# Optimization experiments

Measured on AMD Instinct MI355X. Metric: run time of the kernel, lower is better.

## Reference

```python
import jax, jax.numpy as jnp
import numpy as np

K = 4          # neighbors
R = 2          # step_ratio
OUT = 64       # output_size

def knn_idx(x, k):
    # x: (B, C, N) -> indices of k nearest neighbors (incl. self): (B, N, k)
    xx = jnp.sum(x * x, axis=1)                       # (B, N)
    inner = jnp.einsum('bcn,bcm->bnm', x, x)          # (B, N, N)
    neg_dist = 2.0 * inner - xx[:, :, None] - xx[:, None, :]
    _, idx = jax.lax.top_k(neg_dist, k)               # largest neg_dist = nearest
    return idx

def setup_inputs() -> dict:
    key = jax.random.key(0)
    ks = jax.random.split(key, 7)
    B, C, N = 16, 64, 2048
    s = 0.05
    return {
        'x':  jax.random.normal(ks[0], (B, C, N), jnp.float32),
        'w1': jax.random.normal(ks[1], (OUT, 2 * C), jnp.float32) * s,
        'b1': jax.random.normal(ks[2], (OUT,), jnp.float32) * s,
        'w2': jax.random.normal(ks[3], (OUT * R, 2 * C + OUT), jnp.float32) * s,
        'b2': jax.random.normal(ks[4], (OUT * R,), jnp.float32) * s,
        'w3': jax.random.normal(ks[5], (OUT, OUT), jnp.float32) * s,
        'b3': jax.random.normal(ks[6], (OUT,), jnp.float32) * s,
    }

def reference(x, w1, b1, w2, b2, w3, b3):
    B, C, N = x.shape
    idx = knn_idx(x, K)                                # (B, N, K)
    xt = jnp.transpose(x, (0, 2, 1))                   # (B, N, C)
    neighbors = xt[jnp.arange(B)[:, None, None], idx]  # (B, N, K, C)
    center = jnp.broadcast_to(xt[:, :, None, :], neighbors.shape)
    feat = jnp.concatenate([center, neighbors], axis=-1)   # (B, N, K, 2C), minus_center=False
    # get_graph_feature returns (B, 2C, N, K); module permutes to (B, 2C, K, N)
    f = jnp.transpose(feat, (0, 3, 2, 1))              # (B, 2C, K, N)
    e1 = jnp.einsum('oc,bckn->bokn', w1, f) + b1[None, :, None, None]
    e = jax.nn.relu(jnp.concatenate([e1, f], axis=1))  # (B, 2C+OUT, K, N)
    e2 = jax.nn.relu(jnp.einsum('oc,bckn->bokn', w2, e) + b2[None, :, None, None])  # (B, OUT*R, K, N)
    # permute(0,2,3,1) -> (B,K,N,OUT*R), view -> (B,K,N*R,OUT), permute -> (B,OUT,K,N*R)
    e2 = jnp.transpose(e2, (0, 2, 3, 1)).reshape(B, K, N * R, OUT)
    e2 = jnp.transpose(e2, (0, 3, 1, 2))               # (B, OUT, K, N*R)
    e3 = jnp.einsum('oc,bckn->bokn', w3, e2) + b3[None, :, None, None]
    return jnp.max(e3, axis=2)                          # (B, OUT, N*R)
```

## Files before the change

kernel.cpp:

```cpp
#include <hip/hip_runtime.h>
#include <hip/hip_bf16.h>

#define BB 16
#define CC 64
#define NN 2048
#define KK 4
#define NPART 4
#define JPER (NN / NPART)
#define NCAND 32
#define RSTRIDE 80

typedef unsigned short u16;
typedef unsigned int u32;
typedef __attribute__((ext_vector_type(4))) float f32x4;
typedef __attribute__((ext_vector_type(16))) float f32x16;
typedef __attribute__((ext_vector_type(8))) short short8;

__device__ __forceinline__ float bf2f(u16 u) {
    unsigned int x = ((unsigned int)u) << 16;
    float f;
    __builtin_memcpy(&f, &x, 4);
    return f;
}
__device__ __forceinline__ u16 f2bf(float f) {
    __hip_bfloat16 h = __float2bfloat16(f);
    u16 u;
    __builtin_memcpy(&u, &h, 2);
    return u;
}
__device__ __forceinline__ unsigned int pk2(float a, float b) {
    return (unsigned int)f2bf(a) | ((unsigned int)f2bf(b) << 16);
}
__device__ __forceinline__ u32 umx(u32 a, u32 b) { return a > b ? a : b; }
__device__ __forceinline__ u32 umn(u32 a, u32 b) { return a < b ? a : b; }

__global__ __launch_bounds__(256) void k_prep(const float* __restrict__ x,
                                              float* __restrict__ xt,
                                              double* __restrict__ xx64,
                                              u16* __restrict__ xpk) {
    int b = blockIdx.y;
    int n = blockIdx.x * 256 + threadIdx.x;
    const float* xb = x + (size_t)b * CC * NN;
    float v[CC];
    float s = 0.f;
    double s64 = 0.0;
#pragma unroll
    for (int c = 0; c < CC; c++) {
        v[c] = xb[(size_t)c * NN + n];
        s = fmaf(v[c], v[c], s);
        s64 += (double)v[c] * (double)v[c];
    }
    float4* dst = (float4*)(xt + ((size_t)b * NN + n) * CC);
#pragma unroll
    for (int q = 0; q < 16; q++) {
        dst[q] = make_float4(v[4 * q], v[4 * q + 1], v[4 * q + 2], v[4 * q + 3]);
    }
    xx64[b * NN + n] = s64;
    u16* dp = xpk + ((size_t)b * NN + n) * RSTRIDE;
#pragma unroll
    for (int q = 0; q < 8; q++) {
        uint4 u;
        u.x = pk2(v[8 * q], v[8 * q + 1]);
        u.y = pk2(v[8 * q + 2], v[8 * q + 3]);
        u.z = pk2(v[8 * q + 4], v[8 * q + 5]);
        u.w = pk2(v[8 * q + 6], v[8 * q + 7]);
        *(uint4*)(dp + q * 8) = u;
    }
    u16 hi = f2bf(s);
    u16 lo = f2bf(s - bf2f(hi));
    uint4 u8;
    u8.x = (unsigned int)hi | ((unsigned int)lo << 16);
    u8.y = 0x00003F80u;
    u8.z = 0; u8.w = 0;
    *(uint4*)(dp + 64) = u8;
    uint4 z = {0, 0, 0, 0};
    *(uint4*)(dp + 72) = z;
}

__global__ __launch_bounds__(256) void k_wprep(const float* __restrict__ w1,
                                               const float* __restrict__ w2,
                                               const float* __restrict__ w3,
                                               u16* __restrict__ wb1,
                                               u16* __restrict__ wb2,
                                               u16* __restrict__ wb3) {
    int t = blockIdx.x * 256 + threadIdx.x;
    int stride = gridDim.x * 256;
    for (int idx = t; idx < 64 * 128; idx += stride) {
        int o = idx >> 7, k = idx & 127;
        int cb = o >> 4, lr = o & 15, ks = k >> 5, g = (k >> 3) & 3, e = k & 7;
        wb1[((cb * 4 + ks) * 64 + g * 16 + lr) * 8 + e] = f2bf(w1[idx]);
    }
    for (int idx = t; idx < 128 * 192; idx += stride) {
        int o = idx / 192, k = idx - o * 192;
        int cb = o >> 4, lr = o & 15, ks = k >> 5, g = (k >> 3) & 3, e = k & 7;
        wb2[((cb * 6 + ks) * 64 + g * 16 + lr) * 8 + e] = f2bf(w2[idx]);
    }
    for (int idx = t; idx < 64 * 64; idx += stride) {
        int o = idx >> 6, k = idx & 63;
        int cb = o >> 4, lr = o & 15, ks = k >> 5, g = (k >> 3) & 3, e = k & 7;
        wb3[((cb * 2 + ks) * 64 + g * 16 + lr) * 8 + e] = f2bf(w3[idx]);
    }
}

__global__ __launch_bounds__(256) void k_knn3(const u16* __restrict__ xpk,
                                              u16* __restrict__ cand) {
    int ib = blockIdx.x;
    int part = blockIdx.y;
    int b = blockIdx.z;
    int tid = threadIdx.x;
    int i0 = ib * 128;
    int j00 = part * JPER;

    __shared__ u16 Bb[2 * 2 * 10 * 32 * 8];

    int w = tid >> 6, l = tid & 63;
    int lc = l & 31, lh = l >> 5;
    int hb4 = lh * 4;

    short8 ifrag[5];
    {
        const u16* ip = xpk + ((size_t)b * NN + i0 + w * 32 + lc) * RSTRIDE + lh * 8;
#pragma unroll
        for (int ks = 0; ks < 4; ks++) ifrag[ks] = *(const short8*)(ip + ks * 16);
        short8 f4 = {0, 0, 0, 0, 0, 0, 0, 0};
        if (lh == 0) {
            f4[0] = (short)0xBF00;
            f4[1] = (short)0xBF00;
            f4[2] = (short)0x4300;
        }
        ifrag[4] = f4;
    }

    u32 v0 = 0, v1 = 0, v2 = 0, v3 = 0;

#define CE(a, b) { u32 mx_ = umx(a, b); b = umn(a, b); a = mx_; }

#define STAGE(rr, bf)                                                              \
    {                                                                              \
        int jb = j00 + (rr) * 64;                                                  \
        for (int g = tid; g < 640; g += 256) {                                     \
            int rw = g / 10, c = g - rw * 10;                                      \
            uint4 u = *(const uint4*)(xpk + ((size_t)b * NN + jb + rw) * RSTRIDE + \
                                      c * 8);                                      \
            int sub = rw >> 5, r32 = rw & 31;                                      \
            *(uint4*)((char*)Bb + (bf) * 10240 + sub * 5120 + c * 512 +            \
                      ((r32 ^ (c & 7)) * 16)) = u;                                 \
        }                                                                          \
    }

    STAGE(0, 0);

    for (int r = 0; r < JPER / 64; r++) {
        __syncthreads();
        if (r + 1 < JPER / 64) STAGE(r + 1, (r + 1) & 1);

        const char* bufp = (const char*)Bb + (r & 1) * 10240;
        f32x16 acc0, acc1;
#pragma unroll
        for (int e = 0; e < 16; e++) {
            acc0[e] = 0.f;
            acc1[e] = 0.f;
        }
#pragma unroll
        for (int ks = 0; ks < 5; ks++) {
            int c = ks * 2 + lh;
            int boff = c * 512 + ((lc ^ (c & 7)) * 16);
            short8 a0 = *(const short8*)(bufp + boff);
            short8 a1 = *(const short8*)(bufp + 5120 + boff);
            acc0 = __builtin_amdgcn_mfma_f32_32x32x16_bf16(a0, ifrag[ks], acc0, 0, 0, 0);
            acc1 = __builtin_amdgcn_mfma_f32_32x32x16_bf16(a1, ifrag[ks], acc1, 0, 0, 0);
        }
#pragma unroll
        for (int sub = 0; sub < 2; sub++) {
            const f32x16& acc = sub ? acc1 : acc0;
            int jlb = r * 64 + sub * 32 + hb4;
            u32 kk[16];
#pragma unroll
            for (int rg = 0; rg < 16; rg++) {
                u32 u;
                float f = acc[rg];
                __builtin_memcpy(&u, &f, 4);
                int coff = (rg & 3) + 8 * (rg >> 2);
                kk[rg] = (u & ~0x1FFu) | (u32)(jlb + coff);
            }
#pragma unroll
            for (int q = 0; q < 4; q++) {
                int p = q * 4;
                CE(kk[p + 0], kk[p + 2]); CE(kk[p + 1], kk[p + 3]);
                CE(kk[p + 0], kk[p + 1]); CE(kk[p + 2], kk[p + 3]);
                CE(kk[p + 1], kk[p + 2]);
            }
            kk[0] = umx(kk[0], kk[7]); kk[1] = umx(kk[1], kk[6]);
            kk[2] = umx(kk[2], kk[5]); kk[3] = umx(kk[3], kk[4]);
            CE(kk[0], kk[2]); CE(kk[1], kk[3]); CE(kk[0], kk[1]); CE(kk[2], kk[3]);
            kk[8] = umx(kk[8], kk[15]); kk[9] = umx(kk[9], kk[14]);
            kk[10] = umx(kk[10], kk[13]); kk[11] = umx(kk[11], kk[12]);
            CE(kk[8], kk[10]); CE(kk[9], kk[11]); CE(kk[8], kk[9]); CE(kk[10], kk[11]);
            kk[0] = umx(kk[0], kk[11]); kk[1] = umx(kk[1], kk[10]);
            kk[2] = umx(kk[2], kk[9]); kk[3] = umx(kk[3], kk[8]);
            CE(kk[0], kk[2]); CE(kk[1], kk[3]); CE(kk[0], kk[1]); CE(kk[2], kk[3]);
            v0 = umx(v0, kk[3]); v1 = umx(v1, kk[2]);
            v2 = umx(v2, kk[1]); v3 = umx(v3, kk[0]);
            CE(v0, v2); CE(v1, v3); CE(v0, v1); CE(v2, v3);
        }
    }
#undef STAGE
#undef CE

    size_t cb = ((size_t)b * NN + i0 + w * 32 + lc) * NCAND + part * 8 + lh * 4;
    cand[cb + 0] = (u16)(j00 + (v0 & 0x1FF));
    cand[cb + 1] = (u16)(j00 + (v1 & 0x1FF));
    cand[cb + 2] = (u16)(j00 + (v2 & 0x1FF));
    cand[cb + 3] = (u16)(j00 + (v3 & 0x1FF));
}

__global__ __launch_bounds__(256) void k_knn_merge(const float* __restrict__ xt,
                                                   const double* __restrict__ xx64,
                                                   const u16* __restrict__ cand,
                                                   int* __restrict__ nidx) {
    __shared__ double sv[16 * 33];
    __shared__ u16 ji[16 * 33];

    int tid = threadIdx.x;
    int g = tid >> 4;
    int q = tid & 15;
    size_t gp0 = (size_t)blockIdx.x * 16;
    size_t bbase = (gp0 >> 11) << 11;

    for (int idx = tid; idx < 16 * 32; idx += 256) {
        int p = idx >> 5, c = idx & 31;
        ji[p * 33 + c] = cand[(gp0 + p) * NCAND + c];
    }
    __syncthreads();

    float4 a = ((const float4*)(xt + (gp0 + g) * CC))[q];

    for (int c0 = 0; c0 < NCAND; c0 += 4) {
        int j0 = ji[g * 33 + c0 + 0];
        int j1 = ji[g * 33 + c0 + 1];
        int j2 = ji[g * 33 + c0 + 2];
        int j3 = ji[g * 33 + c0 + 3];
        float4 b0 = ((const float4*)(xt + (bbase + j0) * CC))[q];
        float4 b1 = ((const float4*)(xt + (bbase + j1) * CC))[q];
        float4 b2 = ((const float4*)(xt + (bbase + j2) * CC))[q];
        float4 b3 = ((const float4*)(xt + (bbase + j3) * CC))[q];
        double d0 = (double)a.x * b0.x + (double)a.y * b0.y +
                    (double)a.z * b0.z + (double)a.w * b0.w;
        double d1 = (double)a.x * b1.x + (double)a.y * b1.y +
                    (double)a.z * b1.z + (double)a.w * b1.w;
        double d2 = (double)a.x * b2.x + (double)a.y * b2.y +
                    (double)a.z * b2.z + (double)a.w * b2.w;
        double d3 = (double)a.x * b3.x + (double)a.y * b3.y +
                    (double)a.z * b3.z + (double)a.w * b3.w;
        d0 += __shfl_xor(d0, 8); d1 += __shfl_xor(d1, 8);
        d2 += __shfl_xor(d2, 8); d3 += __shfl_xor(d3, 8);
        d0 += __shfl_xor(d0, 4); d1 += __shfl_xor(d1, 4);
        d2 += __shfl_xor(d2, 4); d3 += __shfl_xor(d3, 4);
        d0 += __shfl_xor(d0, 2); d1 += __shfl_xor(d1, 2);
        d2 += __shfl_xor(d2, 2); d3 += __shfl_xor(d3, 2);
        d0 += __shfl_xor(d0, 1); d1 += __shfl_xor(d1, 1);
        d2 += __shfl_xor(d2, 1); d3 += __shfl_xor(d3, 1);
        if (q == 0) {
            sv[g * 33 + c0 + 0] = 2.0 * d0 - xx64[bbase + j0];
            sv[g * 33 + c0 + 1] = 2.0 * d1 - xx64[bbase + j1];
            sv[g * 33 + c0 + 2] = 2.0 * d2 - xx64[bbase + j2];
            sv[g * 33 + c0 + 3] = 2.0 * d3 - xx64[bbase + j3];
        }
    }
    __syncthreads();

    if (tid < 16) {
        int p = tid;
        double v4[4];
        int id4[4];
#pragma unroll
        for (int s = 0; s < 4; s++) {
            v4[s] = -1e300;
            id4[s] = 0x7fffffff;
        }
        for (int cc = 0; cc < NCAND; cc++) {
            double cv = sv[p * 33 + cc];
            int ci = ji[p * 33 + cc];
#pragma unroll
            for (int s = 0; s < 4; s++) {
                bool take = (cv > v4[s]) || (cv == v4[s] && ci < id4[s]);
                double nv = take ? cv : v4[s];
                int ni = take ? ci : id4[s];
                double ov = take ? v4[s] : cv;
                int oi = take ? id4[s] : ci;
                v4[s] = nv;
                id4[s] = ni;
                cv = ov;
                ci = oi;
            }
        }
        size_t gp2 = gp0 + p;
#pragma unroll
        for (int s = 0; s < 4; s++) nidx[gp2 * 4 + s] = id4[s];
    }
}

__global__ __launch_bounds__(256) void k_mlp(const u16* __restrict__ xpk,
                                             const int* __restrict__ nidx,
                                             const u16* __restrict__ wb1,
                                             const u16* __restrict__ wb2,
                                             const u16* __restrict__ wb3,
                                             const float* __restrict__ b1,
                                             const float* __restrict__ b2,
                                             const float* __restrict__ b3,
                                             float* __restrict__ out) {
    int nch = blockIdx.x;
    int b = blockIdx.y;
    int n0 = nch * 16;
    int tid = threadIdx.x;

    __shared__ u16 Fb[64 * 128];
    __shared__ u16 E1b[64 * 64];
    __shared__ u16 E2b[64 * 128];
    __shared__ float Ob[64 * 36];
    __shared__ int ji[64];

    if (tid < 64) ji[tid] = nidx[((size_t)b * NN + n0) * KK + tid];
    __syncthreads();

    for (int g = tid; g < 64 * 16; g += 256) {
        int it = g >> 4, q = g & 15;
        int half = q >> 3, cq = q & 7;
        int srcn = half ? ji[it] : (n0 + (it >> 2));
        uint4 u = *(const uint4*)(xpk + ((size_t)b * NN + srcn) * RSTRIDE + cq * 8);
        int byte = (it * 256 + half * 128 + cq * 16) ^ ((it & 7) << 4);
        *(uint4*)((char*)Fb + byte) = u;
    }
    __syncthreads();

    int w = tid >> 6, l = tid & 63;
    int lr = l & 15, lg = l >> 4;

    {
        f32x4 acc[4];
#pragma unroll
        for (int g = 0; g < 4; g++) acc[g] = (f32x4){0.f, 0.f, 0.f, 0.f};
#pragma unroll
        for (int ks = 0; ks < 4; ks++) {
            short8 bw = *(const short8*)(wb1 + ((size_t)(w * 4 + ks) * 64 + l) * 8);
#pragma unroll
            for (int g = 0; g < 4; g++) {
                int arow = g * 16 + lr;
                int off = (arow * 256 + ks * 64 + lg * 16) ^ ((arow & 7) << 4);
                short8 a = *(const short8*)((const char*)Fb + off);
                acc[g] = __builtin_amdgcn_mfma_f32_16x16x32_bf16(a, bw, acc[g], 0, 0, 0);
            }
        }
        float bias = b1[w * 16 + lr];
#pragma unroll
        for (int g = 0; g < 4; g++) {
#pragma unroll
            for (int q = 0; q < 4; q++) {
                int item = g * 16 + lg * 4 + q;
                float vv = fmaxf(acc[g][q] + bias, 0.f);
                int byte = (item * 128 + (w * 16 + lr) * 2) ^ ((item & 7) << 4);
                *(u16*)((char*)E1b + byte) = f2bf(vv);
            }
        }
    }
    __syncthreads();

    {
        f32x4 acc[4][2];
#pragma unroll
        for (int g = 0; g < 4; g++)
#pragma unroll
            for (int c2 = 0; c2 < 2; c2++) acc[g][c2] = (f32x4){0.f, 0.f, 0.f, 0.f};
#pragma unroll
        for (int ks = 0; ks < 6; ks++) {
            short8 bw0 = *(const short8*)(wb2 + ((size_t)((w * 2) * 6 + ks) * 64 + l) * 8);
            short8 bw1 = *(const short8*)(wb2 + ((size_t)((w * 2 + 1) * 6 + ks) * 64 + l) * 8);
#pragma unroll
            for (int g = 0; g < 4; g++) {
                int arow = g * 16 + lr;
                int aswz = (arow & 7) << 4;
                short8 a;
                if (ks < 2) {
                    int off = (arow * 128 + ks * 64 + lg * 16) ^ aswz;
                    a = *(const short8*)((const char*)E1b + off);
                } else {
                    int off = (arow * 256 + (ks - 2) * 64 + lg * 16) ^ aswz;
                    uint4 u = *(const uint4*)((const char*)Fb + off);
                    unsigned int m;
                    m = ((u.x >> 15) & 0x10001u) * 0xFFFFu; u.x &= ~m;
                    m = ((u.y >> 15) & 0x10001u) * 0xFFFFu; u.y &= ~m;
                    m = ((u.z >> 15) & 0x10001u) * 0xFFFFu; u.z &= ~m;
                    m = ((u.w >> 15) & 0x10001u) * 0xFFFFu; u.w &= ~m;
                    __builtin_memcpy(&a, &u, 16);
                }
                acc[g][0] = __builtin_amdgcn_mfma_f32_16x16x32_bf16(a, bw0, acc[g][0], 0, 0, 0);
                acc[g][1] = __builtin_amdgcn_mfma_f32_16x16x32_bf16(a, bw1, acc[g][1], 0, 0, 0);
            }
        }
#pragma unroll
        for (int c2 = 0; c2 < 2; c2++) {
            float bias = b2[(w * 2 + c2) * 16 + lr];
#pragma unroll
            for (int g = 0; g < 4; g++) {
#pragma unroll
                for (int q = 0; q < 4; q++) {
                    int item = g * 16 + lg * 4 + q;
                    float vv = fmaxf(acc[g][c2][q] + bias, 0.f);
                    int byte = (item * 256 + ((w * 2 + c2) * 16 + lr) * 2) ^ ((item & 7) << 4);
                    *(u16*)((char*)E2b + byte) = f2bf(vv);
                }
            }
        }
    }
    __syncthreads();

    {
        f32x4 acc[4][2];
#pragma unroll
        for (int g = 0; g < 4; g++)
#pragma unroll
            for (int r = 0; r < 2; r++) acc[g][r] = (f32x4){0.f, 0.f, 0.f, 0.f};
#pragma unroll
        for (int ks = 0; ks < 2; ks++) {
            short8 bw = *(const short8*)(wb3 + ((size_t)(w * 2 + ks) * 64 + l) * 8);
#pragma unroll
            for (int g = 0; g < 4; g++) {
                int arow = g * 16 + lr;
                int aswz = (arow & 7) << 4;
#pragma unroll
                for (int r = 0; r < 2; r++) {
                    int off = (arow * 256 + r * 128 + ks * 64 + lg * 16) ^ aswz;
                    short8 a = *(const short8*)((const char*)E2b + off);
                    acc[g][r] = __builtin_amdgcn_mfma_f32_16x16x32_bf16(a, bw, acc[g][r], 0, 0, 0);
                }
            }
        }
        float bias = b3[w * 16 + lr];
        int o = w * 16 + lr;
#pragma unroll
        for (int g = 0; g < 4; g++) {
            int nl = g * 4 + lg;
#pragma unroll
            for (int r = 0; r < 2; r++) {
                float m = fmaxf(fmaxf(acc[g][r][0], acc[g][r][1]),
                                fmaxf(acc[g][r][2], acc[g][r][3])) + bias;
                Ob[o * 36 + nl * 2 + r] = m;
            }
        }
    }
    __syncthreads();

    {
        int o = tid >> 2, q = tid & 3;
        float4 v0 = *(const float4*)&Ob[o * 36 + q * 8];
        float4 v1 = *(const float4*)&Ob[o * 36 + q * 8 + 4];
        float* dst = out + ((size_t)(b * 64 + o)) * 4096 + n0 * 2 + q * 8;
        ((float4*)dst)[0] = v0;
        ((float4*)dst)[1] = v1;
    }
}

extern "C" void kernel_launch(void* const* d_in, const int* in_sizes, int n_in,
                              void* d_out, int out_size, void* d_ws, size_t ws_size,
                              hipStream_t stream) {
    const float* x = (const float*)d_in[0];
    const float* w1 = (const float*)d_in[1];
    const float* b1 = (const float*)d_in[2];
    const float* w2 = (const float*)d_in[3];
    const float* b2 = (const float*)d_in[4];
    const float* w3 = (const float*)d_in[5];
    const float* b3 = (const float*)d_in[6];
    float* out = (float*)d_out;

    float* xt = (float*)d_ws;
    u16* xpk = (u16*)(xt + (size_t)BB * NN * CC);
    double* xx64 = (double*)(xpk + (size_t)BB * NN * RSTRIDE);
    int* nidx = (int*)(xx64 + (size_t)BB * NN);
    u16* cand = (u16*)(nidx + (size_t)BB * NN * KK);
    u16* wb1 = cand + (size_t)BB * NN * NCAND;
    u16* wb2 = wb1 + 64 * 128;
    u16* wb3 = wb2 + 128 * 192;

    k_prep<<<dim3(NN / 256, BB), 256, 0, stream>>>(x, xt, xx64, xpk);
    k_wprep<<<dim3(32), 256, 0, stream>>>(w1, w2, w3, wb1, wb2, wb3);
    k_knn3<<<dim3(NN / 128, NPART, BB), 256, 0, stream>>>(xpk, cand);
    k_knn_merge<<<dim3(BB * NN / 16), 256, 0, stream>>>(xt, xx64, cand, nidx);
    k_mlp<<<dim3(NN / 16, BB), 256, 0, stream>>>(xpk, nidx, wb1, wb2, wb3, b1, b2, b3, out);
}
```

Baseline: 114.9 us.

## Fuse kNN candidate merge into MLP kernel and swizzle block order

The separate kNN merge kernel is folded into the start of the MLP kernel. Each block refines its own 16 points' candidates in double precision, reusing the Fb shared buffer for the scratch values, and keeps the final 4 neighbor indices in shared memory. This removes one kernel launch and the global round trip through the nidx buffer. The block index is also remapped so that consecutive blocks spread across batches, which may change cache locality. In exchange, the MLP blocks now carry the merge's latency-bound gather and the single-threaded top-4 selection serially before their MLP work.

```diff
diff --git a/kernel.cpp b/kernel.cpp
--- a/kernel.cpp
+++ b/kernel.cpp
@@ -214,119 +214,116 @@
     cand[cb + 3] = (u16)(j00 + (v3 & 0x1FF));
 }
 
-__global__ __launch_bounds__(256) void k_knn_merge(const float* __restrict__ xt,
-                                                   const double* __restrict__ xx64,
-                                                   const u16* __restrict__ cand,
-                                                   int* __restrict__ nidx) {
-    __shared__ double sv[16 * 33];
-    __shared__ u16 ji[16 * 33];
-
+__global__ __launch_bounds__(256) void k_mmlp(const float* __restrict__ xt,
+                                              const double* __restrict__ xx64,
+                                              const u16* __restrict__ cand,
+                                              const u16* __restrict__ xpk,
+                                              const u16* __restrict__ wb1,
+                                              const u16* __restrict__ wb2,
+                                              const u16* __restrict__ wb3,
+                                              const float* __restrict__ b1,
+                                              const float* __restrict__ b2,
+                                              const float* __restrict__ b3,
+                                              float* __restrict__ out) {
     int tid = threadIdx.x;
-    int g = tid >> 4;
-    int q = tid & 15;
-    size_t gp0 = (size_t)blockIdx.x * 16;
-    size_t bbase = (gp0 >> 11) << 11;
-
-    for (int idx = tid; idx < 16 * 32; idx += 256) {
-        int p = idx >> 5, c = idx & 31;
-        ji[p * 33 + c] = cand[(gp0 + p) * NCAND + c];
-    }
-    __syncthreads();
-
-    float4 a = ((const float4*)(xt + (gp0 + g) * CC))[q];
-
-    for (int c0 = 0; c0 < NCAND; c0 += 4) {
-        int j0 = ji[g * 33 + c0 + 0];
-        int j1 = ji[g * 33 + c0 + 1];
-        int j2 = ji[g * 33 + c0 + 2];
-        int j3 = ji[g * 33 + c0 + 3];
-        float4 b0 = ((const float4*)(xt + (bbase + j0) * CC))[q];
-        float4 b1 = ((const float4*)(xt + (bbase + j1) * CC))[q];
-        float4 b2 = ((const float4*)(xt + (bbase + j2) * CC))[q];
-        float4 b3 = ((const float4*)(xt + (bbase + j3) * CC))[q];
-        double d0 = (double)a.x * b0.x + (double)a.y * b0.y +
-                    (double)a.z * b0.z + (double)a.w * b0.w;
-        double d1 = (double)a.x * b1.x + (double)a.y * b1.y +
-                    (double)a.z * b1.z + (double)a.w * b1.w;
-        double d2 = (double)a.x * b2.x + (double)a.y * b2.y +
-                    (double)a.z * b2.z + (double)a.w * b2.w;
-        double d3 = (double)a.x * b3.x + (double)a.y * b3.y +
-                    (double)a.z * b3.z + (double)a.w * b3.w;
-        d0 += __shfl_xor(d0, 8); d1 += __shfl_xor(d1, 8);
-        d2 += __shfl_xor(d2, 8); d3 += __shfl_xor(d3, 8);
-        d0 += __shfl_xor(d0, 4); d1 += __shfl_xor(d1, 4);
-        d2 += __shfl_xor(d2, 4); d3 += __shfl_xor(d3, 4);
-        d0 += __shfl_xor(d0, 2); d1 += __shfl_xor(d1, 2);
-        d2 += __shfl_xor(d2, 2); d3 += __shfl_xor(d3, 2);
-        d0 += __shfl_xor(d0, 1); d1 += __shfl_xor(d1, 1);
-        d2 += __shfl_xor(d2, 1); d3 += __shfl_xor(d3, 1);
-        if (q == 0) {
-            sv[g * 33 + c0 + 0] = 2.0 * d0 - xx64[bbase + j0];
-            sv[g * 33 + c0 + 1] = 2.0 * d1 - xx64[bbase + j1];
-            sv[g * 33 + c0 + 2] = 2.0 * d2 - xx64[bbase + j2];
-            sv[g * 33 + c0 + 3] = 2.0 * d3 - xx64[bbase + j3];
-        }
-    }
-    __syncthreads();
-
-    if (tid < 16) {
-        int p = tid;
-        double v4[4];
-        int id4[4];
-#pragma unroll
-        for (int s = 0; s < 4; s++) {
-            v4[s] = -1e300;
-            id4[s] = 0x7fffffff;
-        }
-        for (int cc = 0; cc < NCAND; cc++) {
-            double cv = sv[p * 33 + cc];
-            int ci = ji[p * 33 + cc];
-#pragma unroll
-            for (int s = 0; s < 4; s++) {
-                bool take = (cv > v4[s]) || (cv == v4[s] && ci < id4[s]);
-                double nv = take ? cv : v4[s];
-                int ni = take ? ci : id4[s];
-                double ov = take ? v4[s] : cv;
-                int oi = take ? id4[s] : ci;
-                v4[s] = nv;
-                id4[s] = ni;
-                cv = ov;
-                ci = oi;
-            }
-        }
-        size_t gp2 = gp0 + p;
-#pragma unroll
-        for (int s = 0; s < 4; s++) nidx[gp2 * 4 + s] = id4[s];
-    }
-}
-
-__global__ __launch_bounds__(256) void k_mlp(const u16* __restrict__ xpk,
-                                             const int* __restrict__ nidx,
-                                             const u16* __restrict__ wb1,
-                                             const u16* __restrict__ wb2,
-                                             const u16* __restrict__ wb3,
-                                             const float* __restrict__ b1,
-                                             const float* __restrict__ b2,
-                                             const float* __restrict__ b3,
-                                             float* __restrict__ out) {
-    int nch = blockIdx.x;
-    int b = blockIdx.y;
+    int lin = blockIdx.y * 128 + blockIdx.x;
+    int swz = (lin & 7) * 256 + (lin >> 3);
+    int b = swz >> 7;
+    int nch = swz & 127;
     int n0 = nch * 16;
-    int tid = threadIdx.x;
-
-    __shared__ u16 Fb[64 * 128];
+
+    __shared__ __align__(16) u16 Fb[64 * 128];
     __shared__ u16 E1b[64 * 64];
     __shared__ u16 E2b[64 * 128];
     __shared__ float Ob[64 * 36];
-    __shared__ int ji[64];
-
-    if (tid < 64) ji[tid] = nidx[((size_t)b * NN + n0) * KK + tid];
+    __shared__ int ji4[64];
+
+    double* sv = (double*)Fb;
+    u16* jc = (u16*)((char*)Fb + 16 * 33 * 8);
+
+    size_t gp0 = (size_t)b * NN + n0;
+    size_t bbase = (size_t)b * NN;
+
+    {
+        int g = tid >> 4;
+        int q = tid & 15;
+        for (int idx = tid; idx < 16 * 32; idx += 256) {
+            int p = idx >> 5, c = idx & 31;
+            jc[p * 33 + c] = cand[(gp0 + p) * NCAND + c];
+        }
+        __syncthreads();
+
+        float4 a = ((const float4*)(xt + (gp0 + g) * CC))[q];
+
+        for (int c0 = 0; c0 < NCAND; c0 += 4) {
+            int j0 = jc[g * 33 + c0 + 0];
+            int j1 = jc[g * 33 + c0 + 1];
+            int j2 = jc[g * 33 + c0 + 2];
+            int j3 = jc[g * 33 + c0 + 3];
+            float4 b0 = ((const float4*)(xt + (bbase + j0) * CC))[q];
+            float4 b1v = ((const float4*)(xt + (bbase + j1) * CC))[q];
+            float4 b2v = ((const float4*)(xt + (bbase + j2) * CC))[q];
+            float4 b3v = ((const float4*)(xt + (bbase + j3) * CC))[q];
+            double d0 = (double)a.x * b0.x + (double)a.y * b0.y +
+                        (double)a.z * b0.z + (double)a.w * b0.w;
+            double d1 = (double)a.x * b1v.x + (double)a.y * b1v.y +
+                        (double)a.z * b1v.z + (double)a.w * b1v.w;
+            double d2 = (double)a.x * b2v.x + (double)a.y * b2v.y +
+                        (double)a.z * b2v.z + (double)a.w * b2v.w;
+            double d3 = (double)a.x * b3v.x + (double)a.y * b3v.y +
+                        (double)a.z * b3v.z + (double)a.w * b3v.w;
+            d0 += __shfl_xor(d0, 8); d1 += __shfl_xor(d1, 8);
+            d2 += __shfl_xor(d2, 8); d3 += __shfl_xor(d3, 8);
+            d0 += __shfl_xor(d0, 4); d1 += __shfl_xor(d1, 4);
+            d2 += __shfl_xor(d2, 4); d3 += __shfl_xor(d3, 4);
+            d0 += __shfl_xor(d0, 2); d1 += __shfl_xor(d1, 2);
+            d2 += __shfl_xor(d2, 2); d3 += __shfl_xor(d3, 2);
+            d0 += __shfl_xor(d0, 1); d1 += __shfl_xor(d1, 1);
+            d2 += __shfl_xor(d2, 1); d3 += __shfl_xor(d3, 1);
+            if (q == 0) {
+                sv[g * 33 + c0 + 0] = 2.0 * d0 - xx64[bbase + j0];
+                sv[g * 33 + c0 + 1] = 2.0 * d1 - xx64[bbase + j1];
+                sv[g * 33 + c0 + 2] = 2.0 * d2 - xx64[bbase + j2];
+                sv[g * 33 + c0 + 3] = 2.0 * d3 - xx64[bbase + j3];
+            }
+        }
+        __syncthreads();
+
+        if (tid < 16) {
+            int p = tid;
+            double v4[4];
+            int id4[4];
+#pragma unroll
+            for (int s = 0; s < 4; s++) {
+                v4[s] = -1e300;
+                id4[s] = 0x7fffffff;
+            }
+            for (int cc = 0; cc < NCAND; cc++) {
+                double cv = sv[p * 33 + cc];
+                int ci = jc[p * 33 + cc];
+#pragma unroll
+                for (int s = 0; s < 4; s++) {
+                    bool take = (cv > v4[s]) || (cv == v4[s] && ci < id4[s]);
+                    double nv = take ? cv : v4[s];
+                    int ni = take ? ci : id4[s];
+                    double ov = take ? v4[s] : cv;
+                    int oi = take ? id4[s] : ci;
+                    v4[s] = nv;
+                    id4[s] = ni;
+                    cv = ov;
+                    ci = oi;
+                }
+            }
+#pragma unroll
+            for (int s = 0; s < 4; s++) ji4[p * 4 + s] = id4[s];
+        }
+    }
     __syncthreads();
 
     for (int g = tid; g < 64 * 16; g += 256) {
         int it = g >> 4, q = g & 15;
         int half = q >> 3, cq = q & 7;
-        int srcn = half ? ji[it] : (n0 + (it >> 2));
+        int srcn = half ? ji4[it] : (n0 + (it >> 2));
         uint4 u = *(const uint4*)(xpk + ((size_t)b * NN + srcn) * RSTRIDE + cq * 8);
         int byte = (it * 256 + half * 128 + cq * 16) ^ ((it & 7) << 4);
         *(uint4*)((char*)Fb + byte) = u;
@@ -475,8 +472,7 @@
     float* xt = (float*)d_ws;
     u16* xpk = (u16*)(xt + (size_t)BB * NN * CC);
     double* xx64 = (double*)(xpk + (size_t)BB * NN * RSTRIDE);
-    int* nidx = (int*)(xx64 + (size_t)BB * NN);
-    u16* cand = (u16*)(nidx + (size_t)BB * NN * KK);
+    u16* cand = (u16*)(xx64 + (size_t)BB * NN);
     u16* wb1 = cand + (size_t)BB * NN * NCAND;
     u16* wb2 = wb1 + 64 * 128;
     u16* wb3 = wb2 + 128 * 192;
@@ -484,6 +480,6 @@
     k_prep<<<dim3(NN / 256, BB), 256, 0, stream>>>(x, xt, xx64, xpk);
     k_wprep<<<dim3(32), 256, 0, stream>>>(w1, w2, w3, wb1, wb2, wb3);
     k_knn3<<<dim3(NN / 128, NPART, BB), 256, 0, stream>>>(xpk, cand);
-    k_knn_merge<<<dim3(BB * NN / 16), 256, 0, stream>>>(xt, xx64, cand, nidx);
-    k_mlp<<<dim3(NN / 16, BB), 256, 0, stream>>>(xpk, nidx, wb1, wb2, wb3, b1, b2, b3, out);
-}
+    k_mmlp<<<dim3(NN / 16, BB), 256, 0, stream>>>(xt, xx64, cand, xpk,
+                                                  wb1, wb2, wb3, b1, b2, b3, out);
+}
```

Result: slower. 124.0 us (+7.9%).
